# Optimization experiments

Hardware: AMD Instinct MI355X
Metric: run time of the kernel (lower is better)

Reference implementation:

```python
import jax, jax.numpy as jnp
import numpy as np

B, N, C, HEADS, P, H, W, TC, ITERS = 2, 4, 128, 8, 4, 96, 96, 64, 3
HD = C // HEADS  # 16
SHIFTS = [(0, 0), (-1, 0), (1, 0), (0, -1), (0, 1)]  # (dx, dy)


def conv1x1(x, w, b):
    # x [B,C,H,W], w [O,C], b [O]
    return jnp.einsum('bchw,oc->bohw', x, w) + b[None, :, None, None]


def grid_sample_bilinear(v, grid):
    # v [M,C,H,W]; grid [M,H,W,2] (x,y) in [-1,1]; align_corners=True, border padding
    M, Cc, Hh, Ww = v.shape
    ix = (grid[..., 0] + 1.0) * 0.5 * (Ww - 1)
    iy = (grid[..., 1] + 1.0) * 0.5 * (Hh - 1)
    x0 = jnp.floor(ix); y0 = jnp.floor(iy)
    wx = (ix - x0)[:, None]; wy = (iy - y0)[:, None]  # [M,1,H,W]
    x0i = jnp.clip(x0, 0, Ww - 1).astype(jnp.int32)
    x1i = jnp.clip(x0 + 1, 0, Ww - 1).astype(jnp.int32)
    y0i = jnp.clip(y0, 0, Hh - 1).astype(jnp.int32)
    y1i = jnp.clip(y0 + 1, 0, Hh - 1).astype(jnp.int32)
    vf = v.reshape(M, Cc, Hh * Ww)
    def gather(yi, xi):
        idx = (yi * Ww + xi).reshape(M, 1, Hh * Ww)
        return jnp.take_along_axis(vf, idx, axis=2).reshape(M, Cc, Hh, Ww)
    return (gather(y0i, x0i) * (1 - wx) * (1 - wy)
            + gather(y0i, x1i) * wx * (1 - wy)
            + gather(y1i, x0i) * (1 - wx) * wy
            + gather(y1i, x1i) * wx * wy)


def gru_cell(x, h, wih, whh, bih, bhh):
    gi = x @ wih.T + bih
    gh = h @ whh.T + bhh
    ir, iz, in_ = jnp.split(gi, 3, axis=-1)
    hr, hz, hn = jnp.split(gh, 3, axis=-1)
    r = jax.nn.sigmoid(ir + hr)
    z = jax.nn.sigmoid(iz + hz)
    n = jnp.tanh(in_ + r * hn)
    return (1.0 - z) * n + z * h


def _correlation_offsets(q, vn):
    # q, vn: [B,HEADS,HD,H,W]
    offset_vals = jnp.asarray(np.array(SHIFTS, dtype=np.float32))  # [5,2] (dx,dy)
    scores = []
    for dx, dy in SHIFTS:
        vs = jnp.roll(vn, shift=(dy, dx), axis=(-2, -1))
        if dy > 0: vs = vs.at[..., :dy, :].set(0.0)
        if dy < 0: vs = vs.at[..., dy:, :].set(0.0)
        if dx > 0: vs = vs.at[..., :, :dx].set(0.0)
        if dx < 0: vs = vs.at[..., :, dx:].set(0.0)
        scores.append((q * vs).sum(axis=2))  # [B,HEADS,H,W]
    best = jnp.argmax(jnp.stack(scores, axis=-1), axis=-1)  # [B,HEADS,H,W]
    bo = offset_vals[best]  # [B,HEADS,H,W,2]
    return jnp.stack([bo[..., 1] * (2.0 / W), bo[..., 0] * (2.0 / H)], axis=-1)


def _forward(query, values, rel_time, time_enc, qw, qb, vw, vb, dww, dwb, pww, pwb,
             wih, whh, bih, bhh, offw, offb, aw, ab, tw, tb, o1w, o1b, o2w, o2b, gate):
    q = conv1x1(query, qw, qb)
    v = conv1x1(values.reshape(B * N, C, H, W), vw, vb).reshape(B, N, C, H, W)
    q_heads = q.reshape(B, HEADS, HD, H, W)
    v_heads = v.reshape(B, N, HEADS, HD, H, W)

    # cnet: depthwise 7x7 -> GELU -> 1x1
    net = jax.lax.conv_general_dilated(query, dww, (1, 1), ((3, 3), (3, 3)),
                                       feature_group_count=C,
                                       dimension_numbers=('NCHW', 'OIHW', 'NCHW'))
    net = jax.nn.gelu(net + dwb[None, :, None, None], approximate=False)
    net = conv1x1(net, pww, pwb)
    net = net.reshape(B, HEADS, HD, H, W).transpose(0, 1, 3, 4, 2).reshape(-1, HD)

    nearest_idx = jnp.argmin(jnp.abs(rel_time), axis=1)  # [B]
    v_nearest = v_heads[jnp.arange(B), nearest_idx]  # [B,HEADS,HD,H,W]

    best_offset = _correlation_offsets(q_heads, v_nearest)  # [B,HEADS,H,W,2]
    curr_offsets = jnp.repeat(best_offset[:, :, :, :, None, :], P, axis=4)
    curr_attn = jnp.zeros((B, HEADS, H, W, N, P), jnp.float32)

    gy, gx = jnp.meshgrid(jnp.linspace(-1.0, 1.0, H), jnp.linspace(-1.0, 1.0, W), indexing='ij')
    base_grid = jnp.stack([gx, gy], axis=-1)  # [H,W,2]

    v_flat = v_nearest.reshape(B * HEADS, HD, H, W)
    for _ in range(ITERS):
        p0 = curr_offsets[..., 0, :]  # [B,HEADS,H,W,2]
        sg = jnp.clip((base_grid[None, None] + p0).reshape(B * HEADS, H, W, 2), -1.0, 1.0)
        sampled = grid_sample_bilinear(v_flat, sg)  # [B*HEADS,HD,H,W]
        sampled = sampled.transpose(0, 2, 3, 1).reshape(-1, HD)
        gru_in = jnp.concatenate([sampled, p0.reshape(-1, 2)], axis=-1)
        net = gru_cell(gru_in, net, wih, whh, bih, bhh)
        d_off = (net @ offw.T + offb).reshape(B, HEADS, H, W, P, 2)
        d_attn = (net @ aw.T + ab).reshape(B, HEADS, H, W, P)
        curr_offsets = curr_offsets + d_off
        curr_attn = curr_attn + d_attn[:, :, :, :, None, :]

    t_bias = (time_enc @ tw.T + tb).transpose(0, 2, 1).reshape(B, HEADS, 1, 1, N, 1)
    final_attn = curr_attn + t_bias
    attn_w = jax.nn.softmax(final_attn.reshape(B, HEADS, H, W, N * P), axis=-1)
    attn_w = attn_w.reshape(B, HEADS, H, W, N, P)

    # deformable sampling over all frames/points, vectorized via vmap
    grids = jnp.clip(base_grid[None, None, :, :, None, :] + curr_offsets, -1.0, 1.0)
    grids = grids.transpose(4, 0, 1, 2, 3, 5).reshape(P, B * HEADS, H, W, 2)
    v_all = v_heads.transpose(1, 0, 2, 3, 4, 5).reshape(N, B * HEADS, HD, H, W)
    samples = jax.vmap(lambda vn: jax.vmap(lambda g: grid_sample_bilinear(vn, g))(grids))(v_all)
    samples = samples.reshape(N, P, B, HEADS, HD, H, W)
    out = jnp.einsum('npbhcyx,bhyxnp->bhcyx', samples, attn_w).reshape(B, C, H, W)

    out = conv1x1(out, o1w, o1b)
    out = jax.nn.gelu(out, approximate=False)
    out = conv1x1(out, o2w, o2b) * jax.nn.sigmoid(gate)

    af = attn_w.reshape(B, HEADS, H, W, N * P)
    entropy = -(af * jnp.log(af + 1e-8)).sum(axis=-1).mean(axis=1, keepdims=True)
    max_ent = float(np.log(N * P))
    confidence = 1.0 - jnp.clip(entropy / (max_ent + 1e-8), 0.0, 1.0)
    return out, confidence, entropy


def setup_inputs():
    key = jax.random.key(0)
    ks = jax.random.split(key, 30)
    def nrm(k, shape, s=1.0):
        return jax.random.normal(k, shape, jnp.float32) * s
    s = 0.05
    return {
        'query': nrm(ks[0], (B, C, H, W)),
        'values': nrm(ks[1], (B, N, C, H, W)),
        'rel_time': nrm(ks[2], (B, N)),
        'time_enc': nrm(ks[3], (B, N, TC)),
        'qw': nrm(ks[4], (C, C), s), 'qb': nrm(ks[5], (C,), s),
        'vw': nrm(ks[6], (C, C), s), 'vb': nrm(ks[7], (C,), s),
        'dww': nrm(ks[8], (C, 1, 7, 7), s), 'dwb': nrm(ks[9], (C,), s),
        'pww': nrm(ks[10], (C, C), s), 'pwb': nrm(ks[11], (C,), s),
        'wih': nrm(ks[12], (3 * HD, HD + 2), s), 'whh': nrm(ks[13], (3 * HD, HD), s),
        'bih': nrm(ks[14], (3 * HD,), s), 'bhh': nrm(ks[15], (3 * HD,), s),
        'offw': nrm(ks[16], (P * 2, HD), s), 'offb': nrm(ks[17], (P * 2,), s),
        'aw': nrm(ks[18], (P, HD), s), 'ab': nrm(ks[19], (P,), s),
        'tw': nrm(ks[20], (HEADS, TC), s), 'tb': nrm(ks[21], (HEADS,), s),
        'o1w': nrm(ks[22], (C, C), s), 'o1b': nrm(ks[23], (C,), s),
        'o2w': nrm(ks[24], (C, C), s), 'o2b': nrm(ks[25], (C,), s),
        'gate': nrm(ks[26], (1, C, 1, 1), s),
    }


def reference(query, values, rel_time, time_enc, qw, qb, vw, vb, dww, dwb, pww, pwb,
              wih, whh, bih, bhh, offw, offb, aw, ab, tw, tb, o1w, o1b, o2w, o2b, gate):
    return _forward(query, values, rel_time, time_enc, qw, qb, vw, vb, dww, dwb, pww, pwb,
                    wih, whh, bih, bhh, offw, offb, aw, ab, tw, tb, o1w, o1b, o2w, o2b, gate)
```

## Files before the change

kernel.cpp:

```cpp
#include <hip/hip_runtime.h>
#include <hip/hip_bf16.h>

typedef unsigned short u16;
typedef unsigned int   u32;

constexpr int kHW = 9216;
constexpr int kM  = 147456;

__device__ __forceinline__ float gelu_f(float v){ return 0.5f*v*(1.0f+erff(v*0.70710678118654752f)); }
__device__ __forceinline__ float sigm_f(float v){ return 1.0f/(1.0f+expf(-v)); }
__device__ __forceinline__ u16 f2bf(float f){
  u32 x = __float_as_uint(f);
  return (u16)((x + 0x7fffu + ((x>>16)&1u)) >> 16);
}
__device__ __forceinline__ int nearest_n(const float* __restrict__ relt, int b){
  int nidx = 0; float bv = fabsf(relt[b*4]);
  for (int n = 1; n < 4; ++n){ float a = fabsf(relt[b*4+n]); if (a < bv){ bv=a; nidx=n; } }
  return nidx;
}

struct Bilin { int i00,i10,i01,i11; float w00,w10,w01,w11; };

__device__ __forceinline__ Bilin make_bilin(int x, int y, float ox, float oy){
  float gx = fmaf((float)x, 2.0f/95.0f, -1.0f);
  float gy = fmaf((float)y, 2.0f/95.0f, -1.0f);
  float sgx = fminf(fmaxf(gx+ox,-1.0f),1.0f);
  float sgy = fminf(fmaxf(gy+oy,-1.0f),1.0f);
  float ix = (sgx+1.0f)*0.5f*95.0f;
  float iy = (sgy+1.0f)*0.5f*95.0f;
  float x0f = floorf(ix), y0f = floorf(iy);
  float wx = ix-x0f, wy = iy-y0f;
  int x0 = min(max((int)x0f,0),95), y0 = min(max((int)y0f,0),95);
  int x1 = min(x0+1,95), y1 = min(y0+1,95);
  Bilin b;
  b.i00=(y0*96+x0)*16; b.i10=(y0*96+x1)*16; b.i01=(y1*96+x0)*16; b.i11=(y1*96+x1)*16;
  float iwx=1.0f-wx, iwy=1.0f-wy;
  b.w00=iwx*iwy; b.w10=wx*iwy; b.w01=iwx*wy; b.w11=wx*wy;
  return b;
}

__device__ __forceinline__ void sample16(const float* __restrict__ vp, const Bilin& bl, float* __restrict__ o){
  const float4* p00 = (const float4*)(vp + bl.i00);
  const float4* p10 = (const float4*)(vp + bl.i10);
  const float4* p01 = (const float4*)(vp + bl.i01);
  const float4* p11 = (const float4*)(vp + bl.i11);
  #pragma unroll
  for (int g = 0; g < 4; ++g){
    float4 a=p00[g], b=p10[g], c=p01[g], d=p11[g];
    o[g*4+0] = a.x*bl.w00 + b.x*bl.w10 + c.x*bl.w01 + d.x*bl.w11;
    o[g*4+1] = a.y*bl.w00 + b.y*bl.w10 + c.y*bl.w01 + d.y*bl.w11;
    o[g*4+2] = a.z*bl.w00 + b.z*bl.w10 + c.z*bl.w01 + d.z*bl.w11;
    o[g*4+3] = a.w*bl.w00 + b.w*bl.w10 + c.w*bl.w01 + d.w*bl.w11;
  }
}

__global__ __launch_bounds__(256) void prep_k(const float* __restrict__ qw, const float* __restrict__ vw,
    const float* __restrict__ pww, const float* __restrict__ o1w, const float* __restrict__ o2w,
    float* __restrict__ wt)
{
  const float* src = (blockIdx.y==0)?qw:(blockIdx.y==1)?vw:(blockIdx.y==2)?pww:(blockIdx.y==3)?o1w:o2w;
  float* d = wt + blockIdx.y*16384;
  int i = blockIdx.x*256 + threadIdx.x;
  int o = i & 127, c = i >> 7;
  d[i] = src[o*128 + c];
}

template<int ASRC, int EPI>
__global__ __launch_bounds__(256, 3) void gemm1x1_k(const void* __restrict__ inp,
    const float* __restrict__ wt, const float* __restrict__ bias,
    float* __restrict__ outf, u16* __restrict__ out16,
    const float* __restrict__ gate, const float* __restrict__ relt)
{
  __shared__ __align__(16) float a_s[16*132];
  __shared__ __align__(16) float b_s[16*132];
  const int tid = threadIdx.x;
  const int tx = tid & 15, ty = tid >> 4;
  const int img = blockIdx.y;
  const int px0 = blockIdx.x * 128;
  const int sr = tid >> 4;
  const int sc = (tid & 15) * 8;

  float acc[64];
  #pragma unroll
  for (int oj = 0; oj < 8; ++oj) {
    float bv = bias[tx*8+oj];
    #pragma unroll
    for (int pi = 0; pi < 8; ++pi) acc[pi*8+oj] = bv;
  }

  for (int kc = 0; kc < 8; ++kc) {
    const int k0 = kc*16;
    { const float4* g = (const float4*)(wt + (k0+sr)*128 + sc);
      float4 v0 = g[0], v1 = g[1];
      *(float4*)&b_s[sr*132+sc] = v0; *(float4*)&b_s[sr*132+sc+4] = v1; }
    if (ASRC == 0) {
      const float* inf = (const float*)inp;
      const float4* g = (const float4*)(inf + (size_t)(img*128 + k0 + sr)*kHW + px0 + sc);
      float4 v0 = g[0], v1 = g[1];
      *(float4*)&a_s[sr*132+sc] = v0; *(float4*)&a_s[sr*132+sc+4] = v1;
    } else {
      const u16* g16 = (const u16*)inp;
      const int px = tid >> 1, hd0 = (tid & 1)*8;
      uint4 raw = *(const uint4*)(g16 + ((size_t)(img*8 + kc)*kHW + px0 + px)*16 + hd0);
      u32 w[4] = {raw.x, raw.y, raw.z, raw.w};
      #pragma unroll
      for (int gi = 0; gi < 4; ++gi) {
        a_s[(hd0+gi*2+0)*132+px] = __uint_as_float(w[gi]<<16);
        a_s[(hd0+gi*2+1)*132+px] = __uint_as_float(w[gi]&0xffff0000u);
      }
    }
    __syncthreads();
    #pragma unroll
    for (int k = 0; k < 16; ++k) {
      float4 b0 = *(const float4*)&b_s[k*132 + tx*8];
      float4 b1 = *(const float4*)&b_s[k*132 + tx*8 + 4];
      float4 a0 = *(const float4*)&a_s[k*132 + ty*8];
      float4 a1 = *(const float4*)&a_s[k*132 + ty*8 + 4];
      float av[8] = {a0.x,a0.y,a0.z,a0.w,a1.x,a1.y,a1.z,a1.w};
      float bv[8] = {b0.x,b0.y,b0.z,b0.w,b1.x,b1.y,b1.z,b1.w};
      #pragma unroll
      for (int pi = 0; pi < 8; ++pi)
        #pragma unroll
        for (int oj = 0; oj < 8; ++oj)
          acc[pi*8+oj] = fmaf(av[pi], bv[oj], acc[pi*8+oj]);
    }
    __syncthreads();
  }

  if (EPI == 0) {
    const int head = tx >> 1, hd0 = (tx & 1)*8;
    #pragma unroll
    for (int pi = 0; pi < 8; ++pi) {
      const int px = px0 + ty*8 + pi;
      float* dst = outf + ((size_t)(img*8 + head)*kHW + px)*16 + hd0;
      float4 t0 = {acc[pi*8+0],acc[pi*8+1],acc[pi*8+2],acc[pi*8+3]};
      float4 t1 = {acc[pi*8+4],acc[pi*8+5],acc[pi*8+6],acc[pi*8+7]};
      *(float4*)dst = t0; *(float4*)(dst+4) = t1;
    }
  } else if (EPI == 3) {
    const int b = img >> 2, n = img & 3;
    const int nidx = nearest_n(relt, b);
    const int head = tx >> 1, hd0 = (tx & 1)*8;
    #pragma unroll
    for (int pi = 0; pi < 8; ++pi) {
      const int px = px0 + ty*8 + pi;
      u16* d16 = out16 + ((size_t)(img*8 + head)*kHW + px)*16 + hd0;
      uint4 packed;
      packed.x = (u32)f2bf(acc[pi*8+0]) | ((u32)f2bf(acc[pi*8+1])<<16);
      packed.y = (u32)f2bf(acc[pi*8+2]) | ((u32)f2bf(acc[pi*8+3])<<16);
      packed.z = (u32)f2bf(acc[pi*8+4]) | ((u32)f2bf(acc[pi*8+5])<<16);
      packed.w = (u32)f2bf(acc[pi*8+6]) | ((u32)f2bf(acc[pi*8+7])<<16);
      *(uint4*)d16 = packed;
      if (n == nidx) {
        float* dst = outf + ((size_t)(b*8 + head)*kHW + px)*16 + hd0;
        float4 t0 = {acc[pi*8+0],acc[pi*8+1],acc[pi*8+2],acc[pi*8+3]};
        float4 t1 = {acc[pi*8+4],acc[pi*8+5],acc[pi*8+6],acc[pi*8+7]};
        *(float4*)dst = t0; *(float4*)(dst+4) = t1;
      }
    }
  } else {
    #pragma unroll
    for (int oj = 0; oj < 8; ++oj) {
      const int o = tx*8 + oj;
      float* dst = outf + (size_t)(img*128 + o)*kHW + px0 + ty*8;
      float v[8];
      #pragma unroll
      for (int pi = 0; pi < 8; ++pi) {
        float t = acc[pi*8+oj];
        v[pi] = (EPI == 1) ? gelu_f(t) : t * sigm_f(gate[o]);
      }
      float4 t0 = {v[0],v[1],v[2],v[3]};
      float4 t1 = {v[4],v[5],v[6],v[7]};
      *(float4*)dst = t0; *(float4*)(dst+4) = t1;
    }
  }
}

__global__ __launch_bounds__(256) void dw_k(const float* __restrict__ q, const float* __restrict__ dww,
    const float* __restrict__ dwb, float* __restrict__ outf)
{
  int idx = blockIdx.x*256 + threadIdx.x;
  int px = idx % kHW;
  int bc = idx / kHW;
  int c = bc & 127;
  int x = px % 96, y = px / 96;
  float s = dwb[c];
  const float* qb = q + (size_t)bc*kHW;
  #pragma unroll
  for (int ky = 0; ky < 7; ++ky) {
    int yy = y + ky - 3;
    if (yy < 0 || yy > 95) continue;
    #pragma unroll
    for (int kx = 0; kx < 7; ++kx) {
      int xx = x + kx - 3;
      if (xx < 0 || xx > 95) continue;
      s = fmaf(qb[yy*96+xx], dww[c*49 + ky*7 + kx], s);
    }
  }
  outf[idx] = gelu_f(s);
}

__global__ void tb_k(const float* __restrict__ te, const float* __restrict__ tw,
                     const float* __restrict__ tbias, float* __restrict__ tbb)
{
  int i = threadIdx.x;
  if (i >= 64) return;
  int b = i >> 5, h = (i >> 2) & 7, n = i & 3;
  float s = tbias[h];
  for (int tc = 0; tc < 64; ++tc) s = fmaf(te[(b*4+n)*64 + tc], tw[h*64+tc], s);
  tbb[(b*8+h)*4 + n] = s;
}

__global__ __launch_bounds__(256) void fused_k(
    const float* __restrict__ qb, const float* __restrict__ vf32, const u16* __restrict__ vb16,
    const float* __restrict__ netb, const float* __restrict__ relt,
    const float* __restrict__ wih, const float* __restrict__ whh,
    const float* __restrict__ bihp, const float* __restrict__ bhhp,
    const float* __restrict__ offw, const float* __restrict__ offbp,
    const float* __restrict__ aw, const float* __restrict__ abp,
    const float* __restrict__ tbb,
    u16* __restrict__ outattn16, float* __restrict__ entb)
{
  __shared__ __align__(16) float s_wih[48*20];
  __shared__ __align__(16) float s_whh[48*16];
  __shared__ __align__(16) float s_offw[8*16];
  __shared__ __align__(16) float s_aw[4*16];
  __shared__ float s_bih[48], s_bhh[48], s_offb[8], s_ab[4];
  const int tid = threadIdx.x;
  for (int i = tid; i < 960; i += 256){ int g = i/20, k = i%20; s_wih[i] = (k<18)? wih[g*18+k] : 0.0f; }
  for (int i = tid; i < 768; i += 256) s_whh[i] = whh[i];
  if (tid < 128) s_offw[tid] = offw[tid];
  if (tid < 64)  s_aw[tid]  = aw[tid];
  if (tid < 48){ s_bih[tid] = bihp[tid]; s_bhh[tid] = bhhp[tid]; }
  if (tid < 8)   s_offb[tid] = offbp[tid];
  if (tid < 4)   s_ab[tid]  = abp[tid];

  const int vblk = (blockIdx.x & 7)*72 + (blockIdx.x >> 3);
  const int item = vblk*256 + tid;
  const int yx = item % kHW; const int bh = item / kHW;
  const int b = bh >> 3, head = bh & 7;
  const int x = yx % 96, y = yx / 96;
  const float* vp = vf32 + (size_t)(b*8 + head)*kM;

  float off_[8], attn_[4];
  {
    float qv[16];
    { const float4* q4 = (const float4*)(qb + (size_t)bh*kM + yx*16);
      #pragma unroll
      for (int g = 0; g < 4; ++g){ float4 t = q4[g]; qv[g*4]=t.x; qv[g*4+1]=t.y; qv[g*4+2]=t.z; qv[g*4+3]=t.w; } }
    const int sdx[5] = {0,-1,1,0,0};
    const int sdy[5] = {0,0,0,-1,1};
    float4 tv[5][4]; bool valid[5];
    #pragma unroll
    for (int s5 = 0; s5 < 5; ++s5) {
      int sy = y - sdy[s5], sx = x - sdx[s5];
      valid[s5] = (sy >= 0 && sy < 96 && sx >= 0 && sx < 96);
      int syc = min(max(sy,0),95), sxc = min(max(sx,0),95);
      const float4* tp = (const float4*)(vp + (syc*96+sxc)*16);
      tv[s5][0] = tp[0]; tv[s5][1] = tp[1]; tv[s5][2] = tp[2]; tv[s5][3] = tp[3];
    }
    double bsc = 0.0; int best = 0;
    #pragma unroll
    for (int s5 = 0; s5 < 5; ++s5) {
      double sc = 0.0;
      if (valid[s5]) {
        const float* tp = (const float*)&tv[s5][0];
        #pragma unroll
        for (int hd = 0; hd < 16; ++hd) sc += (double)qv[hd]*(double)tp[hd];
      }
      if (s5 == 0) { bsc = sc; best = 0; }
      else if (sc > bsc) { bsc = sc; best = s5; }
    }
    const float STEP = 2.0f/96.0f;
    float ox = 0.f, oy = 0.f;
    if (best == 3) ox = -STEP; else if (best == 4) ox = STEP;
    if (best == 1) oy = -STEP; else if (best == 2) oy = STEP;
    #pragma unroll
    for (int p = 0; p < 4; ++p) { off_[2*p] = ox; off_[2*p+1] = oy; attn_[p] = 0.0f; }
  }

  float h[16];
  { const float4* n4 = (const float4*)(netb + (size_t)item*16);
    #pragma unroll
    for (int g = 0; g < 4; ++g){ float4 t = n4[g]; h[g*4]=t.x; h[g*4+1]=t.y; h[g*4+2]=t.z; h[g*4+3]=t.w; } }

  __syncthreads();

  for (int it = 0; it < 3; ++it) {
    const float p0x = off_[0];
    const float p0y = off_[1];
    Bilin bl = make_bilin(x, y, p0x, p0y);
    float xv[20];
    sample16(vp, bl, xv);
    xv[16] = p0x; xv[17] = p0y; xv[18] = 0.f; xv[19] = 0.f;

    float hn[16];
    #pragma unroll 2
    for (int j = 0; j < 16; ++j) {
      float g0 = s_bih[j], g1 = s_bih[16+j], g2 = s_bih[32+j];
      const float4* w0r = (const float4*)&s_wih[j*20];
      const float4* w1r = (const float4*)&s_wih[(16+j)*20];
      const float4* w2r = (const float4*)&s_wih[(32+j)*20];
      #pragma unroll
      for (int q4 = 0; q4 < 5; ++q4) {
        float4 w0 = w0r[q4], w1 = w1r[q4], w2 = w2r[q4];
        float a0 = xv[q4*4+0], a1 = xv[q4*4+1], a2 = xv[q4*4+2], a3 = xv[q4*4+3];
        g0 = fmaf(a0,w0.x,g0); g0 = fmaf(a1,w0.y,g0); g0 = fmaf(a2,w0.z,g0); g0 = fmaf(a3,w0.w,g0);
        g1 = fmaf(a0,w1.x,g1); g1 = fmaf(a1,w1.y,g1); g1 = fmaf(a2,w1.z,g1); g1 = fmaf(a3,w1.w,g1);
        g2 = fmaf(a0,w2.x,g2); g2 = fmaf(a1,w2.y,g2); g2 = fmaf(a2,w2.z,g2); g2 = fmaf(a3,w2.w,g2);
      }
      float t0 = s_bhh[j], t1 = s_bhh[16+j], t2 = s_bhh[32+j];
      const float4* h0r = (const float4*)&s_whh[j*16];
      const float4* h1r = (const float4*)&s_whh[(16+j)*16];
      const float4* h2r = (const float4*)&s_whh[(32+j)*16];
      #pragma unroll
      for (int q4 = 0; q4 < 4; ++q4) {
        float4 w0 = h0r[q4], w1 = h1r[q4], w2 = h2r[q4];
        float a0 = h[q4*4+0], a1 = h[q4*4+1], a2 = h[q4*4+2], a3 = h[q4*4+3];
        t0 = fmaf(a0,w0.x,t0); t0 = fmaf(a1,w0.y,t0); t0 = fmaf(a2,w0.z,t0); t0 = fmaf(a3,w0.w,t0);
        t1 = fmaf(a0,w1.x,t1); t1 = fmaf(a1,w1.y,t1); t1 = fmaf(a2,w1.z,t1); t1 = fmaf(a3,w1.w,t1);
        t2 = fmaf(a0,w2.x,t2); t2 = fmaf(a1,w2.y,t2); t2 = fmaf(a2,w2.z,t2); t2 = fmaf(a3,w2.w,t2);
      }
      float r = sigm_f(g0 + t0);
      float z = sigm_f(g1 + t1);
      float nn = tanhf(fmaf(r, t2, g2));
      hn[j] = fmaf(z, h[j], (1.0f - z)*nn);
    }
    #pragma unroll
    for (int j = 0; j < 16; ++j) h[j] = hn[j];

    #pragma unroll
    for (int d = 0; d < 8; ++d) {
      const float4* wr = (const float4*)&s_offw[d*16];
      float s = s_offb[d];
      #pragma unroll
      for (int q4 = 0; q4 < 4; ++q4) {
        float4 w4 = wr[q4];
        s = fmaf(h[q4*4+0], w4.x, s); s = fmaf(h[q4*4+1], w4.y, s);
        s = fmaf(h[q4*4+2], w4.z, s); s = fmaf(h[q4*4+3], w4.w, s);
      }
      off_[d] += s;
    }
    #pragma unroll
    for (int p = 0; p < 4; ++p) {
      const float4* wr = (const float4*)&s_aw[p*16];
      float s = s_ab[p];
      #pragma unroll
      for (int q4 = 0; q4 < 4; ++q4) {
        float4 w4 = wr[q4];
        s = fmaf(h[q4*4+0], w4.x, s); s = fmaf(h[q4*4+1], w4.y, s);
        s = fmaf(h[q4*4+2], w4.z, s); s = fmaf(h[q4*4+3], w4.w, s);
      }
      attn_[p] += s;
    }
  }

  float lg[16];
  #pragma unroll
  for (int n = 0; n < 4; ++n) {
    float tv2 = tbb[(b*8+head)*4 + n];
    #pragma unroll
    for (int p = 0; p < 4; ++p) lg[n*4+p] = attn_[p] + tv2;
  }
  float mx = lg[0];
  #pragma unroll
  for (int i = 1; i < 16; ++i) mx = fmaxf(mx, lg[i]);
  float es = 0.f;
  #pragma unroll
  for (int i = 0; i < 16; ++i){ lg[i] = expf(lg[i]-mx); es += lg[i]; }
  float inv = 1.0f/es;
  float ent = 0.f;
  #pragma unroll
  for (int i = 0; i < 16; ++i){ lg[i] *= inv; ent -= lg[i]*logf(lg[i] + 1e-8f); }
  entb[item] = ent;

  float acc[16];
  #pragma unroll
  for (int j = 0; j < 16; ++j) acc[j] = 0.f;
  #pragma unroll
  for (int p = 0; p < 4; ++p) {
    Bilin bl = make_bilin(x, y, off_[2*p], off_[2*p+1]);
    uint4 raw[4][8];
    #pragma unroll
    for (int n = 0; n < 4; ++n) {
      const u16* vpn = vb16 + (size_t)((b*4+n)*8 + head)*kM;
      raw[n][0] = *(const uint4*)(vpn + bl.i00); raw[n][1] = *(const uint4*)(vpn + bl.i00 + 8);
      raw[n][2] = *(const uint4*)(vpn + bl.i10); raw[n][3] = *(const uint4*)(vpn + bl.i10 + 8);
      raw[n][4] = *(const uint4*)(vpn + bl.i01); raw[n][5] = *(const uint4*)(vpn + bl.i01 + 8);
      raw[n][6] = *(const uint4*)(vpn + bl.i11); raw[n][7] = *(const uint4*)(vpn + bl.i11 + 8);
    }
    #pragma unroll
    for (int n = 0; n < 4; ++n) {
      u32 aw2[8] = {raw[n][0].x,raw[n][0].y,raw[n][0].z,raw[n][0].w, raw[n][1].x,raw[n][1].y,raw[n][1].z,raw[n][1].w};
      u32 bw2[8] = {raw[n][2].x,raw[n][2].y,raw[n][2].z,raw[n][2].w, raw[n][3].x,raw[n][3].y,raw[n][3].z,raw[n][3].w};
      u32 cw2[8] = {raw[n][4].x,raw[n][4].y,raw[n][4].z,raw[n][4].w, raw[n][5].x,raw[n][5].y,raw[n][5].z,raw[n][5].w};
      u32 dw2[8] = {raw[n][6].x,raw[n][6].y,raw[n][6].z,raw[n][6].w, raw[n][7].x,raw[n][7].y,raw[n][7].z,raw[n][7].w};
      float wnp = lg[n*4+p];
      #pragma unroll
      for (int g = 0; g < 8; ++g){
        float alo = __uint_as_float(aw2[g]<<16), ahi = __uint_as_float(aw2[g]&0xffff0000u);
        float blo = __uint_as_float(bw2[g]<<16), bhi = __uint_as_float(bw2[g]&0xffff0000u);
        float clo = __uint_as_float(cw2[g]<<16), chi = __uint_as_float(cw2[g]&0xffff0000u);
        float dlo = __uint_as_float(dw2[g]<<16), dhi = __uint_as_float(dw2[g]&0xffff0000u);
        float s0 = alo*bl.w00 + blo*bl.w10 + clo*bl.w01 + dlo*bl.w11;
        float s1 = ahi*bl.w00 + bhi*bl.w10 + chi*bl.w01 + dhi*bl.w11;
        acc[g*2+0] = fmaf(wnp, s0, acc[g*2+0]);
        acc[g*2+1] = fmaf(wnp, s1, acc[g*2+1]);
      }
    }
  }
  uint4 pk0, pk1;
  pk0.x = (u32)f2bf(acc[0])  | ((u32)f2bf(acc[1])<<16);
  pk0.y = (u32)f2bf(acc[2])  | ((u32)f2bf(acc[3])<<16);
  pk0.z = (u32)f2bf(acc[4])  | ((u32)f2bf(acc[5])<<16);
  pk0.w = (u32)f2bf(acc[6])  | ((u32)f2bf(acc[7])<<16);
  pk1.x = (u32)f2bf(acc[8])  | ((u32)f2bf(acc[9])<<16);
  pk1.y = (u32)f2bf(acc[10]) | ((u32)f2bf(acc[11])<<16);
  pk1.z = (u32)f2bf(acc[12]) | ((u32)f2bf(acc[13])<<16);
  pk1.w = (u32)f2bf(acc[14]) | ((u32)f2bf(acc[15])<<16);
  *(uint4*)(outattn16 + (size_t)item*16)     = pk0;
  *(uint4*)(outattn16 + (size_t)item*16 + 8) = pk1;
}

__global__ __launch_bounds__(256) void ent_k(const float* __restrict__ entb, float* __restrict__ outf)
{
  int idx = blockIdx.x*256 + threadIdx.x;
  int b = idx / kHW, yx = idx % kHW;
  float s = 0.f;
  #pragma unroll
  for (int h8 = 0; h8 < 8; ++h8) s += entb[(b*8+h8)*kHW + yx];
  s *= 0.125f;
  float conf = 1.0f - fminf(fmaxf(s / (2.772588722239781f + 1e-8f), 0.0f), 1.0f);
  outf[2359296 + idx]         = conf;
  outf[2359296 + 18432 + idx] = s;
}

extern "C" void kernel_launch(void* const* d_in, const int* in_sizes, int n_in,
                              void* d_out, int out_size, void* d_ws, size_t ws_size,
                              hipStream_t stream)
{
  const float* query  = (const float*)d_in[0];
  const float* values = (const float*)d_in[1];
  const float* relt   = (const float*)d_in[2];
  const float* time_enc = (const float*)d_in[3];
  const float* qw  = (const float*)d_in[4];
  const float* qb  = (const float*)d_in[5];
  const float* vw  = (const float*)d_in[6];
  const float* vb  = (const float*)d_in[7];
  const float* dww = (const float*)d_in[8];
  const float* dwb = (const float*)d_in[9];
  const float* pww = (const float*)d_in[10];
  const float* pwb = (const float*)d_in[11];
  const float* wih = (const float*)d_in[12];
  const float* whh = (const float*)d_in[13];
  const float* bih = (const float*)d_in[14];
  const float* bhh = (const float*)d_in[15];
  const float* offw = (const float*)d_in[16];
  const float* offb = (const float*)d_in[17];
  const float* aw  = (const float*)d_in[18];
  const float* ab  = (const float*)d_in[19];
  const float* tw  = (const float*)d_in[20];
  const float* tb  = (const float*)d_in[21];
  const float* o1w = (const float*)d_in[22];
  const float* o1b = (const float*)d_in[23];
  const float* o2w = (const float*)d_in[24];
  const float* o2b = (const float*)d_in[25];
  const float* gate = (const float*)d_in[26];
  float* out = (float*)d_out;
  float* ws = (float*)d_ws;

  u16*   vb16   = (u16*)ws;
  float* vf32n  = ws + 4718592;
  float* qbuf   = ws + 7077888;
  float* netb   = ws + 9437184;
  float* dwbuf  = ws + 11796480;
  u16*   oat16  = (u16*)dwbuf;
  float* entbf  = ws + 14155776;
  float* tbbuf  = ws + 14303232;
  float* wtbuf  = ws + 14303360;
  if (ws_size < 14385280ull * 4ull) return;

  float* wt_q  = wtbuf;
  float* wt_v  = wtbuf + 16384;
  float* wt_pw = wtbuf + 32768;
  float* wt_o1 = wtbuf + 49152;
  float* wt_o2 = wtbuf + 65536;

  dim3 blk(256,1,1);
  prep_k<<<dim3(64,5,1), blk, 0, stream>>>(qw, vw, pww, o1w, o2w, wtbuf);
  gemm1x1_k<0,0><<<dim3(72,2,1), blk, 0, stream>>>(query, wt_q, qb, qbuf, nullptr, nullptr, nullptr);
  dw_k<<<dim3(9216,1,1), blk, 0, stream>>>(query, dww, dwb, dwbuf);
  gemm1x1_k<0,0><<<dim3(72,2,1), blk, 0, stream>>>(dwbuf, wt_pw, pwb, netb, nullptr, nullptr, nullptr);
  gemm1x1_k<0,3><<<dim3(72,8,1), blk, 0, stream>>>(values, wt_v, vb, vf32n, vb16, nullptr, relt);
  tb_k<<<dim3(1,1,1), dim3(64,1,1), 0, stream>>>(time_enc, tw, tb, tbbuf);
  fused_k<<<dim3(576,1,1), blk, 0, stream>>>(qbuf, vf32n, vb16, netb, relt,
                                             wih, whh, bih, bhh, offw, offb, aw, ab,
                                             tbbuf, oat16, entbf);
  ent_k<<<dim3(72,1,1), blk, 0, stream>>>(entbf, out);
  gemm1x1_k<2,1><<<dim3(72,2,1), blk, 0, stream>>>(oat16, wt_o1, o1b, qbuf, nullptr, nullptr, nullptr);
  gemm1x1_k<0,2><<<dim3(72,2,1), blk, 0, stream>>>(qbuf, wt_o2, o2b, out, nullptr, gate, nullptr);
}
```

Measured before the change: 469.9 us.

## Merge q/v/pw 1x1 GEMMs into one launch and fuse o1→GELU→o2 via LDS

The three input-side 1x1 convolutions (query, values, depthwise-pointwise) now run in a single grid that picks its source, weight and epilogue from blockIdx.y. This replaces three launches and lets the small grids share the device. The two output projections are fused into one kernel that keeps the GELU intermediate tile in a 66KB shared-memory buffer, which avoids a global write and re-read of the intermediate. The large LDS footprint cuts occupancy of the fused output kernel, and that kernel still runs on only 144 blocks.

```diff
diff --git a/kernel.cpp b/kernel.cpp
--- a/kernel.cpp
+++ b/kernel.cpp
@@ -65,17 +65,22 @@
   d[i] = src[o*128 + c];
 }
 
-template<int ASRC, int EPI>
-__global__ __launch_bounds__(256, 3) void gemm1x1_k(const void* __restrict__ inp,
-    const float* __restrict__ wt, const float* __restrict__ bias,
-    float* __restrict__ outf, u16* __restrict__ out16,
-    const float* __restrict__ gate, const float* __restrict__ relt)
+__global__ __launch_bounds__(256, 3) void gemm_qvp_k(
+    const float* __restrict__ query, const float* __restrict__ values, const float* __restrict__ dwbuf,
+    const float* __restrict__ wtb,
+    const float* __restrict__ qb2, const float* __restrict__ vb2, const float* __restrict__ pwb2,
+    float* __restrict__ qbuf, float* __restrict__ netb,
+    float* __restrict__ vf32n, u16* __restrict__ vb16, const float* __restrict__ relt)
 {
   __shared__ __align__(16) float a_s[16*132];
   __shared__ __align__(16) float b_s[16*132];
   const int tid = threadIdx.x;
   const int tx = tid & 15, ty = tid >> 4;
-  const int img = blockIdx.y;
+  const int iy = blockIdx.y;
+  const float* inp; const float* wt; const float* bias; int img; int mode;
+  if (iy < 2)       { inp = query;  wt = wtb;         bias = qb2;  img = iy;      mode = 0; }
+  else if (iy < 10) { inp = values; wt = wtb + 16384; bias = vb2;  img = iy - 2;  mode = 1; }
+  else              { inp = dwbuf;  wt = wtb + 32768; bias = pwb2; img = iy - 10; mode = 2; }
   const int px0 = blockIdx.x * 128;
   const int sr = tid >> 4;
   const int sc = (tid & 15) * 8;
@@ -93,22 +98,9 @@
     { const float4* g = (const float4*)(wt + (k0+sr)*128 + sc);
       float4 v0 = g[0], v1 = g[1];
       *(float4*)&b_s[sr*132+sc] = v0; *(float4*)&b_s[sr*132+sc+4] = v1; }
-    if (ASRC == 0) {
-      const float* inf = (const float*)inp;
-      const float4* g = (const float4*)(inf + (size_t)(img*128 + k0 + sr)*kHW + px0 + sc);
+    { const float4* g = (const float4*)(inp + (size_t)(img*128 + k0 + sr)*kHW + px0 + sc);
       float4 v0 = g[0], v1 = g[1];
-      *(float4*)&a_s[sr*132+sc] = v0; *(float4*)&a_s[sr*132+sc+4] = v1;
-    } else {
-      const u16* g16 = (const u16*)inp;
-      const int px = tid >> 1, hd0 = (tid & 1)*8;
-      uint4 raw = *(const uint4*)(g16 + ((size_t)(img*8 + kc)*kHW + px0 + px)*16 + hd0);
-      u32 w[4] = {raw.x, raw.y, raw.z, raw.w};
-      #pragma unroll
-      for (int gi = 0; gi < 4; ++gi) {
-        a_s[(hd0+gi*2+0)*132+px] = __uint_as_float(w[gi]<<16);
-        a_s[(hd0+gi*2+1)*132+px] = __uint_as_float(w[gi]&0xffff0000u);
-      }
-    }
+      *(float4*)&a_s[sr*132+sc] = v0; *(float4*)&a_s[sr*132+sc+4] = v1; }
     __syncthreads();
     #pragma unroll
     for (int k = 0; k < 16; ++k) {
@@ -127,24 +119,14 @@
     __syncthreads();
   }
 
-  if (EPI == 0) {
-    const int head = tx >> 1, hd0 = (tx & 1)*8;
+  const int head = tx >> 1, hd0 = (tx & 1)*8;
+  if (mode == 1) {
+    const int b = img >> 2, n = img & 3;
+    const int nidx = nearest_n(relt, b);
     #pragma unroll
     for (int pi = 0; pi < 8; ++pi) {
       const int px = px0 + ty*8 + pi;
-      float* dst = outf + ((size_t)(img*8 + head)*kHW + px)*16 + hd0;
-      float4 t0 = {acc[pi*8+0],acc[pi*8+1],acc[pi*8+2],acc[pi*8+3]};
-      float4 t1 = {acc[pi*8+4],acc[pi*8+5],acc[pi*8+6],acc[pi*8+7]};
-      *(float4*)dst = t0; *(float4*)(dst+4) = t1;
-    }
-  } else if (EPI == 3) {
-    const int b = img >> 2, n = img & 3;
-    const int nidx = nearest_n(relt, b);
-    const int head = tx >> 1, hd0 = (tx & 1)*8;
-    #pragma unroll
-    for (int pi = 0; pi < 8; ++pi) {
-      const int px = px0 + ty*8 + pi;
-      u16* d16 = out16 + ((size_t)(img*8 + head)*kHW + px)*16 + hd0;
+      u16* d16 = vb16 + ((size_t)(img*8 + head)*kHW + px)*16 + hd0;
       uint4 packed;
       packed.x = (u32)f2bf(acc[pi*8+0]) | ((u32)f2bf(acc[pi*8+1])<<16);
       packed.y = (u32)f2bf(acc[pi*8+2]) | ((u32)f2bf(acc[pi*8+3])<<16);
@@ -152,27 +134,124 @@
       packed.w = (u32)f2bf(acc[pi*8+6]) | ((u32)f2bf(acc[pi*8+7])<<16);
       *(uint4*)d16 = packed;
       if (n == nidx) {
-        float* dst = outf + ((size_t)(b*8 + head)*kHW + px)*16 + hd0;
+        float* dst = vf32n + ((size_t)(b*8 + head)*kHW + px)*16 + hd0;
         float4 t0 = {acc[pi*8+0],acc[pi*8+1],acc[pi*8+2],acc[pi*8+3]};
         float4 t1 = {acc[pi*8+4],acc[pi*8+5],acc[pi*8+6],acc[pi*8+7]};
         *(float4*)dst = t0; *(float4*)(dst+4) = t1;
       }
     }
   } else {
-    #pragma unroll
-    for (int oj = 0; oj < 8; ++oj) {
-      const int o = tx*8 + oj;
-      float* dst = outf + (size_t)(img*128 + o)*kHW + px0 + ty*8;
-      float v[8];
-      #pragma unroll
-      for (int pi = 0; pi < 8; ++pi) {
-        float t = acc[pi*8+oj];
-        v[pi] = (EPI == 1) ? gelu_f(t) : t * sigm_f(gate[o]);
-      }
-      float4 t0 = {v[0],v[1],v[2],v[3]};
-      float4 t1 = {v[4],v[5],v[6],v[7]};
+    float* outf = (mode == 0) ? qbuf : netb;
+    #pragma unroll
+    for (int pi = 0; pi < 8; ++pi) {
+      const int px = px0 + ty*8 + pi;
+      float* dst = outf + ((size_t)(img*8 + head)*kHW + px)*16 + hd0;
+      float4 t0 = {acc[pi*8+0],acc[pi*8+1],acc[pi*8+2],acc[pi*8+3]};
+      float4 t1 = {acc[pi*8+4],acc[pi*8+5],acc[pi*8+6],acc[pi*8+7]};
       *(float4*)dst = t0; *(float4*)(dst+4) = t1;
     }
+  }
+}
+
+__global__ __launch_bounds__(256) void o1o2_k(const u16* __restrict__ oat,
+    const float* __restrict__ wt1, const float* __restrict__ o1b,
+    const float* __restrict__ wt2, const float* __restrict__ o2b,
+    const float* __restrict__ gate, float* __restrict__ out)
+{
+  __shared__ __align__(16) float a_s[16*132];
+  __shared__ __align__(16) float b_s[16*132];
+  __shared__ __align__(16) float mid[128*132];
+  const int tid = threadIdx.x;
+  const int tx = tid & 15, ty = tid >> 4;
+  const int img = blockIdx.y;
+  const int px0 = blockIdx.x * 128;
+  const int sr = tid >> 4;
+  const int sc = (tid & 15) * 8;
+
+  float acc[64];
+  #pragma unroll
+  for (int oj = 0; oj < 8; ++oj) {
+    float bv = o1b[tx*8+oj];
+    #pragma unroll
+    for (int pi = 0; pi < 8; ++pi) acc[pi*8+oj] = bv;
+  }
+  for (int kc = 0; kc < 8; ++kc) {
+    const int k0 = kc*16;
+    { const float4* g = (const float4*)(wt1 + (k0+sr)*128 + sc);
+      float4 v0 = g[0], v1 = g[1];
+      *(float4*)&b_s[sr*132+sc] = v0; *(float4*)&b_s[sr*132+sc+4] = v1; }
+    { const int px = tid >> 1, hd0 = (tid & 1)*8;
+      uint4 raw = *(const uint4*)(oat + ((size_t)(img*8 + kc)*kHW + px0 + px)*16 + hd0);
+      u32 w[4] = {raw.x, raw.y, raw.z, raw.w};
+      #pragma unroll
+      for (int gi = 0; gi < 4; ++gi) {
+        a_s[(hd0+gi*2+0)*132+px] = __uint_as_float(w[gi]<<16);
+        a_s[(hd0+gi*2+1)*132+px] = __uint_as_float(w[gi]&0xffff0000u);
+      }
+    }
+    __syncthreads();
+    #pragma unroll
+    for (int k = 0; k < 16; ++k) {
+      float4 b0 = *(const float4*)&b_s[k*132 + tx*8];
+      float4 b1 = *(const float4*)&b_s[k*132 + tx*8 + 4];
+      float4 a0 = *(const float4*)&a_s[k*132 + ty*8];
+      float4 a1 = *(const float4*)&a_s[k*132 + ty*8 + 4];
+      float av[8] = {a0.x,a0.y,a0.z,a0.w,a1.x,a1.y,a1.z,a1.w};
+      float bv[8] = {b0.x,b0.y,b0.z,b0.w,b1.x,b1.y,b1.z,b1.w};
+      #pragma unroll
+      for (int pi = 0; pi < 8; ++pi)
+        #pragma unroll
+        for (int oj = 0; oj < 8; ++oj)
+          acc[pi*8+oj] = fmaf(av[pi], bv[oj], acc[pi*8+oj]);
+    }
+    __syncthreads();
+  }
+  #pragma unroll
+  for (int oj = 0; oj < 8; ++oj)
+    #pragma unroll
+    for (int pi = 0; pi < 8; ++pi)
+      mid[(tx*8+oj)*132 + ty*8+pi] = gelu_f(acc[pi*8+oj]);
+  __syncthreads();
+
+  #pragma unroll
+  for (int oj = 0; oj < 8; ++oj) {
+    float bv = o2b[tx*8+oj];
+    #pragma unroll
+    for (int pi = 0; pi < 8; ++pi) acc[pi*8+oj] = bv;
+  }
+  for (int kc = 0; kc < 8; ++kc) {
+    const int k0 = kc*16;
+    { const float4* g = (const float4*)(wt2 + (k0+sr)*128 + sc);
+      float4 v0 = g[0], v1 = g[1];
+      *(float4*)&b_s[sr*132+sc] = v0; *(float4*)&b_s[sr*132+sc+4] = v1; }
+    __syncthreads();
+    #pragma unroll
+    for (int k = 0; k < 16; ++k) {
+      float4 b0 = *(const float4*)&b_s[k*132 + tx*8];
+      float4 b1 = *(const float4*)&b_s[k*132 + tx*8 + 4];
+      float4 a0 = *(const float4*)&mid[(k0+k)*132 + ty*8];
+      float4 a1 = *(const float4*)&mid[(k0+k)*132 + ty*8 + 4];
+      float av[8] = {a0.x,a0.y,a0.z,a0.w,a1.x,a1.y,a1.z,a1.w};
+      float bv[8] = {b0.x,b0.y,b0.z,b0.w,b1.x,b1.y,b1.z,b1.w};
+      #pragma unroll
+      for (int pi = 0; pi < 8; ++pi)
+        #pragma unroll
+        for (int oj = 0; oj < 8; ++oj)
+          acc[pi*8+oj] = fmaf(av[pi], bv[oj], acc[pi*8+oj]);
+    }
+    __syncthreads();
+  }
+  #pragma unroll
+  for (int oj = 0; oj < 8; ++oj) {
+    const int o = tx*8 + oj;
+    float* dst = out + (size_t)(img*128 + o)*kHW + px0 + ty*8;
+    float sg = sigm_f(gate[o]);
+    float v[8];
+    #pragma unroll
+    for (int pi = 0; pi < 8; ++pi) v[pi] = acc[pi*8+oj] * sg;
+    float4 t0 = {v[0],v[1],v[2],v[3]};
+    float4 t1 = {v[4],v[5],v[6],v[7]};
+    *(float4*)dst = t0; *(float4*)(dst+4) = t1;
   }
 }
 
@@ -480,23 +559,18 @@
   float* wtbuf  = ws + 14303360;
   if (ws_size < 14385280ull * 4ull) return;
 
-  float* wt_q  = wtbuf;
-  float* wt_v  = wtbuf + 16384;
-  float* wt_pw = wtbuf + 32768;
   float* wt_o1 = wtbuf + 49152;
   float* wt_o2 = wtbuf + 65536;
 
   dim3 blk(256,1,1);
   prep_k<<<dim3(64,5,1), blk, 0, stream>>>(qw, vw, pww, o1w, o2w, wtbuf);
-  gemm1x1_k<0,0><<<dim3(72,2,1), blk, 0, stream>>>(query, wt_q, qb, qbuf, nullptr, nullptr, nullptr);
   dw_k<<<dim3(9216,1,1), blk, 0, stream>>>(query, dww, dwb, dwbuf);
-  gemm1x1_k<0,0><<<dim3(72,2,1), blk, 0, stream>>>(dwbuf, wt_pw, pwb, netb, nullptr, nullptr, nullptr);
-  gemm1x1_k<0,3><<<dim3(72,8,1), blk, 0, stream>>>(values, wt_v, vb, vf32n, vb16, nullptr, relt);
+  gemm_qvp_k<<<dim3(72,12,1), blk, 0, stream>>>(query, values, dwbuf, wtbuf,
+                                                qb, vb, pwb, qbuf, netb, vf32n, vb16, relt);
   tb_k<<<dim3(1,1,1), dim3(64,1,1), 0, stream>>>(time_enc, tw, tb, tbbuf);
   fused_k<<<dim3(576,1,1), blk, 0, stream>>>(qbuf, vf32n, vb16, netb, relt,
                                              wih, whh, bih, bhh, offw, offb, aw, ab,
                                              tbbuf, oat16, entbf);
   ent_k<<<dim3(72,1,1), blk, 0, stream>>>(entbf, out);
-  gemm1x1_k<2,1><<<dim3(72,2,1), blk, 0, stream>>>(oat16, wt_o1, o1b, qbuf, nullptr, nullptr, nullptr);
-  gemm1x1_k<0,2><<<dim3(72,2,1), blk, 0, stream>>>(qbuf, wt_o2, o2b, out, nullptr, gate, nullptr);
-}
+  o1o2_k<<<dim3(72,2,1), blk, 0, stream>>>(oat16, wt_o1, o1b, wt_o2, o2b, gate, out);
+}
```

After: 434.8 us. 1.08x faster.
